# Kernel optimization log

Hardware: AMD Instinct MI355X
Metric: run time of the kernel (lower is better)

## Reference

```python
import jax, jax.numpy as jnp
import numpy as np

B, CIN, CH, COUT = 16, 256, 256, 256
RES = 16
E = 32           # embed_dim
NEMB = 1024      # codebook size
NP = 128         # n_phylo_channels (ch - NP == NP)
L = 4            # n_phylolevels
K = 8            # attribute codes per level per kernel
KN = 32          # nonattribute codes per kernel (levels=1)
CP = L * K * E   # 1024 projected phylo channels
CN = KN * E      # 1024 projected nonattr channels
BETA = 0.25
EPS = 1e-5

def conv1x1(x, w, b):
    # x: [B,C,H,W], w: [O,C], b: [O]
    return jnp.einsum('oc,bchw->bohw', w, x) + b[None, :, None, None]

def layernorm_chw(x, w, b):
    # LayerNorm over (C,H,W) per sample, elementwise affine of shape [C,H,W]
    mu = jnp.mean(x, axis=(1, 2, 3), keepdims=True)
    var = jnp.var(x, axis=(1, 2, 3), keepdims=True)
    return (x - mu) * jax.lax.rsqrt(var + EPS) * w[None] + b[None]

def reshape_in(x, levels):
    # [B, E*levels*K', H, W] -> [B, E, K'*H*W, levels]
    Bb, C, H, W = x.shape
    Kp = C // (E * levels)
    x = x.reshape(Bb, E, levels, Kp, H * W)
    x = x.transpose(0, 1, 3, 4, 2)          # [B,E,K',HW,levels]
    return x.reshape(Bb, E, Kp * H * W, levels)

def reshape_out(x, levels):
    # [B, E, K'*HW, levels] -> [B, E*levels*K', RES, RES]
    Bb, Ee, N, Ll = x.shape
    Kp = N // (RES * RES)
    x = x.reshape(Bb, Ee, Kp, RES * RES, Ll)
    x = x.transpose(0, 1, 4, 2, 3)          # [B,E,levels,K',HW]
    return x.reshape(Bb, Ee * Ll * Kp, RES, RES)

def quantize(z, codebook):
    # z: [B, E, N, levels]; codebook: [NEMB, E]
    zp = z.transpose(0, 2, 3, 1)            # [B,N,levels,E]
    flat = zp.reshape(-1, E)
    d = (jnp.sum(flat * flat, axis=1, keepdims=True)
         - 2.0 * flat @ codebook.T
         + jnp.sum(codebook * codebook, axis=1)[None, :])
    idx = jnp.argmin(d, axis=1)
    zq = codebook[idx].reshape(zp.shape)
    sg = jax.lax.stop_gradient
    loss = jnp.mean((sg(zq) - zp) ** 2) + BETA * jnp.mean((zq - sg(zp)) ** 2)
    zq = zp + sg(zq - zp)                   # straight-through
    return zq.transpose(0, 3, 1, 2), loss

def setup_inputs() -> dict:
    key = jax.random.key(0)
    ks = jax.random.split(key, 20)
    s = 0.02
    inp = {
        'x': jax.random.normal(ks[0], (B, CIN, RES, RES), jnp.float32),
        'conv_in_w': jax.random.normal(ks[1], (CH, CIN), jnp.float32) * s,
        'conv_in_b': jnp.zeros((CH,), jnp.float32),
        'ln_p_w': jnp.ones((NP, RES, RES), jnp.float32),
        'ln_p_b': jnp.zeros((NP, RES, RES), jnp.float32),
        'wp_in': jax.random.normal(ks[2], (CP, NP), jnp.float32) * s,
        'bp_in': jnp.zeros((CP,), jnp.float32),
        'wp_out': jax.random.normal(ks[3], (NP, CP), jnp.float32) * s,
        'bp_out': jnp.zeros((NP,), jnp.float32),
        'ln_n_w': jnp.ones((CH - NP, RES, RES), jnp.float32),
        'ln_n_b': jnp.zeros((CH - NP, RES, RES), jnp.float32),
        'wn_in': jax.random.normal(ks[4], (CN, CH - NP), jnp.float32) * s,
        'bn_in': jnp.zeros((CN,), jnp.float32),
        'wn_out': jax.random.normal(ks[5], (CH - NP, CN), jnp.float32) * s,
        'bn_out': jnp.zeros((CH - NP,), jnp.float32),
        'codebook': jax.random.uniform(ks[6], (NEMB, E), jnp.float32,
                                       -1.0 / NEMB, 1.0 / NEMB),
        'conv_out_w': jax.random.normal(ks[7], (COUT, CH), jnp.float32) * s,
        'conv_out_b': jnp.zeros((COUT,), jnp.float32),
    }
    return inp

def reference(x, conv_in_w, conv_in_b, ln_p_w, ln_p_b, wp_in, bp_in,
              wp_out, bp_out, ln_n_w, ln_n_b, wn_in, bn_in, wn_out, bn_out,
              codebook, conv_out_w, conv_out_b):
    silu = jax.nn.silu
    h = conv1x1(silu(x), conv_in_w, conv_in_b)
    h_p, h_n = h[:, :NP], h[:, NP:]
    # phylo branch
    z_p = silu(conv1x1(layernorm_chw(silu(h_p), ln_p_w, ln_p_b), wp_in, bp_in))
    zq_p, loss_p = quantize(reshape_in(z_p, L), codebook)
    hout_p = silu(conv1x1(reshape_out(zq_p, L), wp_out, bp_out))
    # non-attribute branch (anticlassification path)
    z_n = silu(conv1x1(layernorm_chw(silu(h_n), ln_n_w, ln_n_b), wn_in, bn_in))
    zq_n, loss_n = quantize(reshape_in(z_n, 1), codebook)
    hout_n = silu(conv1x1(reshape_out(zq_n, 1), wn_out, bn_out))
    h_cat = jnp.concatenate([hout_p, hout_n], axis=1)
    out = conv1x1(silu(h_cat), conv_out_w, conv_out_b)
    return out, loss_p + loss_n, zq_p
```

## Files before the change

kernel.cpp:

```cpp
#include <hip/hip_runtime.h>
#include <hip/hip_bf16.h>


__device__ __forceinline__ float silu_rw(float x){ return x / (1.f + expf(-x)); }
__device__ __forceinline__ float b2f_rw(__hip_bfloat16 v){ return __bfloat162float(v); }
__device__ __forceinline__ float ldv_rw(const void* p, int i, int f32m){
  if (f32m) return ((const float*)p)[i];
  return b2f_rw(((const __hip_bfloat16*)p)[i]);
}

#define FLAGS_OFF 0
#define LOSS_OFF  4
#define STATS_OFF 8
#define CB32_OFF  128
#define CBN_OFF   32896
#define IDXP_OFF  33984
#define IDXN_OFF  165056
#define R2_OFF    296192
#define R3_OFF    820480
#define R1_OFF    1344768

__global__ __launch_bounds__(256) void detect_rw(const void* cbv, float* flags, float* lossacc){
  __shared__ int bad;
  if (threadIdx.x == 0) bad = 0;
  __syncthreads();
  const unsigned short* u = (const unsigned short*)cbv;
  int local = 0;
  for (int i = threadIdx.x; i < 32768; i += 256){
    unsigned e = (u[i] >> 7) & 0xFF;
    if (e >= 126) local = 1;
  }
  if (local) bad = 1;
  __syncthreads();
  if (threadIdx.x == 0){
    flags[0] = bad ? 1.f : 0.f;
    lossacc[0] = 0.f; lossacc[1] = 0.f;
  }
}

__global__ __launch_bounds__(256) void cbprep_rw(const void* cbv, const float* flags,
                                                 float* cb32, float* cbn){
  const int f32m = (flags[0] != 0.f);
  int j = blockIdx.x * 256 + threadIdx.x;
  if (j < 1024){
    float s = 0.f;
    for (int e = 0; e < 32; ++e){
      float v = ldv_rw(cbv, j*32 + e, f32m);
      cb32[j*32 + e] = v;
      s += v*v;
    }
    cbn[j] = s;
  }
}

template<int KCH, int INMODE, bool OUTSILU, bool ATOMIC, int LEVELS>
__global__ __launch_bounds__(256) void gemm2_rw(
    const float* __restrict__ inF, const float* __restrict__ inF2,
    const void* __restrict__ inV,
    const void* __restrict__ W, const void* __restrict__ biasO,
    const void* __restrict__ sbA, const void* __restrict__ sbB,
    const int* __restrict__ idxin, const float* __restrict__ cb32,
    float* __restrict__ outF, const float* __restrict__ flags,
    int KDIM, int OUTC, int o_off, int b_base, int ib_sub, int ob_sub)
{
  __shared__ float As[32][32];
  __shared__ float Bs[32][68];
  __shared__ int   IdxS[32][32];

  const int f32m = (flags[0] != 0.f);
  const int t  = threadIdx.x;
  const int q0 = (blockIdx.x << 5) + (b_base << 8);
  const int b  = q0 >> 8;
  const int p0 = q0 & 255;
  const int o0 = blockIdx.y << 6;
  const int k0base = blockIdx.z * KCH;
  const int tx = t & 15, ty = t >> 4;
  float acc[4][2] = {};

  const int sch = t >> 3, spx = (t & 7) << 2;

  if constexpr (INMODE == 3){
    #pragma unroll
    for (int j = 0; j < 4; ++j){
      const int p = p0 + spx + j;
      if constexpr (LEVELS == 4){
        const int l = sch >> 3, kp = sch & 7;
        IdxS[sch][spx + j] = idxin[b*8192 + (((kp << 8) + p) << 2) + l];
      } else {
        IdxS[sch][spx + j] = idxin[b*8192 + (sch << 8) + p];
      }
    }
    __syncthreads();
  }

  for (int kc = 0; kc < KCH; kc += 32){
    const int k0 = k0base + kc;
    if constexpr (INMODE == 0){
      const float4 v = *reinterpret_cast<const float4*>(
          &inF[(((b - ib_sub)*KDIM + k0 + sch) << 8) + p0 + spx]);
      *reinterpret_cast<float4*>(&As[sch][spx]) = v;
    } else if constexpr (INMODE == 2){
      if (f32m){
        const float* xf = (const float*)inV;
        float4 v = *reinterpret_cast<const float4*>(&xf[((b*KDIM + k0 + sch) << 8) + p0 + spx]);
        v.x = silu_rw(v.x); v.y = silu_rw(v.y); v.z = silu_rw(v.z); v.w = silu_rw(v.w);
        *reinterpret_cast<float4*>(&As[sch][spx]) = v;
      } else {
        const __hip_bfloat16* xb = (const __hip_bfloat16*)inV;
        const int off = ((b*KDIM + k0 + sch) << 8) + p0 + spx;
        #pragma unroll
        for (int j = 0; j < 4; ++j) As[sch][spx + j] = silu_rw(b2f_rw(xb[off + j]));
      }
    } else if constexpr (INMODE == 3){
      const int e = k0 >> 5;
      #pragma unroll
      for (int j = 0; j < 4; ++j)
        As[sch][spx + j] = cb32[((IdxS[sch][spx + j] & 1023) << 5) + e];
    } else {
      const float* src = (k0 < 128) ? inF : inF2;
      const void* sb   = (k0 < 128) ? sbA : sbB;
      const int kh = k0 & 127;
      const float bb = ldv_rw(sb, kh + sch, f32m);
      float4 v = *reinterpret_cast<const float4*>(&src[((b*128 + kh + sch) << 8) + p0 + spx]);
      v.x = silu_rw(v.x + bb); v.y = silu_rw(v.y + bb);
      v.z = silu_rw(v.z + bb); v.w = silu_rw(v.w + bb);
      *reinterpret_cast<float4*>(&As[sch][spx]) = v;
    }
    if (f32m){
      const float* Wf = (const float*)W;
      #pragma unroll
      for (int r = 0; r < 8; ++r){
        int ii = t + (r << 8); int oo = ii >> 5, cc = ii & 31;
        Bs[cc][oo] = Wf[(o0 + oo)*KDIM + k0 + cc];
      }
    } else {
      const __hip_bfloat16* Wb = (const __hip_bfloat16*)W;
      #pragma unroll
      for (int r = 0; r < 8; ++r){
        int ii = t + (r << 8); int oo = ii >> 5, cc = ii & 31;
        Bs[cc][oo] = b2f_rw(Wb[(o0 + oo)*KDIM + k0 + cc]);
      }
    }
    __syncthreads();
    #pragma unroll
    for (int kk = 0; kk < 32; ++kk){
      const float2 a = *reinterpret_cast<const float2*>(&As[kk][tx << 1]);
      const float4 w = *reinterpret_cast<const float4*>(&Bs[kk][ty << 2]);
      acc[0][0] += w.x*a.x; acc[0][1] += w.x*a.y;
      acc[1][0] += w.y*a.x; acc[1][1] += w.y*a.y;
      acc[2][0] += w.z*a.x; acc[2][1] += w.z*a.y;
      acc[3][0] += w.w*a.x; acc[3][1] += w.w*a.y;
    }
    __syncthreads();
  }
  #pragma unroll
  for (int i = 0; i < 4; ++i){
    const int o = o0 + (ty << 2) + i;
    const int base = (((b - ob_sub)*OUTC + o_off + o) << 8) + p0 + (tx << 1);
    if constexpr (ATOMIC){
      atomicAdd(&outF[base + 0], acc[i][0]);
      atomicAdd(&outF[base + 1], acc[i][1]);
    } else {
      const float bb = ldv_rw(biasO, o, f32m);
      float v0 = acc[i][0] + bb, v1 = acc[i][1] + bb;
      if constexpr (OUTSILU){ v0 = silu_rw(v0); v1 = silu_rw(v1); }
      *reinterpret_cast<float2*>(&outF[base]) = make_float2(v0, v1);
    }
  }
}

__global__ __launch_bounds__(256) void stats_rw(const float* __restrict__ h, float* __restrict__ stats){
  const int b = blockIdx.x >> 1, half = blockIdx.x & 1;
  const float* base = h + ((b*256 + half*128) << 8);
  float s = 0.f, s2 = 0.f;
  for (int i = threadIdx.x; i < 32768; i += 256){
    float a = silu_rw(base[i]);
    s += a; s2 += a*a;
  }
  __shared__ float sh[2][256];
  sh[0][threadIdx.x] = s; sh[1][threadIdx.x] = s2;
  __syncthreads();
  for (int st = 128; st > 0; st >>= 1){
    if (threadIdx.x < st){
      sh[0][threadIdx.x] += sh[0][threadIdx.x + st];
      sh[1][threadIdx.x] += sh[1][threadIdx.x + st];
    }
    __syncthreads();
  }
  if (threadIdx.x == 0){
    float mu  = sh[0][0] * (1.f/32768.f);
    float var = sh[1][0] * (1.f/32768.f) - mu*mu;
    stats[half*32 + b]      = mu;
    stats[half*32 + 16 + b] = 1.f / sqrtf(var + 1e-5f);
  }
}

__global__ __launch_bounds__(256) void ln_rw(const float* __restrict__ h,
    const void* lwp, const void* lbp, const void* lwn, const void* lbn,
    const float* __restrict__ stats, const float* __restrict__ flags,
    float* __restrict__ lnp, float* __restrict__ lnn){
  const int f32m = (flags[0] != 0.f);
  int i = blockIdx.x * 256 + threadIdx.x;
  int b = i >> 16, c = (i >> 8) & 255, p = i & 255;
  float a = silu_rw(h[i]);
  if (c < 128){
    float v = (a - stats[b]) * stats[16 + b] * ldv_rw(lwp, (c << 8) + p, f32m) + ldv_rw(lbp, (c << 8) + p, f32m);
    lnp[((b*128 + c) << 8) + p] = v;
  } else {
    int cc = c - 128;
    float v = (a - stats[32 + b]) * stats[48 + b] * ldv_rw(lwn, (cc << 8) + p, f32m) + ldv_rw(lbn, (cc << 8) + p, f32m);
    lnn[((b*128 + cc) << 8) + p] = v;
  }
}

template<int LEVELS>
__global__ __launch_bounds__(256) void quant_rw(const float* __restrict__ z,
    const float* __restrict__ cb32, const float* __restrict__ cbn,
    int* __restrict__ idxout, float* __restrict__ lossacc, int b_base, int CS){
  __shared__ float4 cbT[2056];
  __shared__ float  cbnS[1056];
  __shared__ float  red[256];

  const int tid = threadIdx.x;
  const int gid = blockIdx.x * 256 + tid;
  const int pt = gid & 7;
  const int vbase = gid >> 3;
  const int halfstride = CS << 12;
  const int vid0 = vbase, vid1 = vbase + halfstride;

  const int bl0 = vid0 >> 13, bl1 = vid1 >> 13;
  const int w = vid0 & 8191;
  int p, cbase;
  if (LEVELS == 4){
    int l = w & 3, n = w >> 2;
    p = n & 255; cbase = (l << 3) + (n >> 8);
  } else {
    p = w & 255; cbase = w >> 8;
  }

  #pragma unroll
  for (int q = 0; q < 4; ++q){
    const int i = tid + (q << 8);
    cbnS[i + (i >> 5)] = cbn[i];
  }

  float4 za[8], zb[8];
  float zn0 = 0.f, zn1 = 0.f;
  const int zoff = ((bl0 << 10) + cbase) << 8;
  const int zoff1 = ((bl1 << 10) + cbase) << 8;
  #pragma unroll
  for (int e4 = 0; e4 < 8; ++e4){
    float4 a, b;
    a.x = z[zoff  + (((e4<<2)+0) << 13) + p];
    a.y = z[zoff  + (((e4<<2)+1) << 13) + p];
    a.z = z[zoff  + (((e4<<2)+2) << 13) + p];
    a.w = z[zoff  + (((e4<<2)+3) << 13) + p];
    b.x = z[zoff1 + (((e4<<2)+0) << 13) + p];
    b.y = z[zoff1 + (((e4<<2)+1) << 13) + p];
    b.z = z[zoff1 + (((e4<<2)+2) << 13) + p];
    b.w = z[zoff1 + (((e4<<2)+3) << 13) + p];
    za[e4] = a; zb[e4] = b;
    zn0 += a.x*a.x; zn0 += a.y*a.y; zn0 += a.z*a.z; zn0 += a.w*a.w;
    zn1 += b.x*b.x; zn1 += b.y*b.y; zn1 += b.z*b.z; zn1 += b.w*b.w;
  }

  float best0 = __builtin_inff(), best1 = __builtin_inff();
  int bi0 = 0, bi1 = 0;

  const int jl0 = pt << 5;
  for (int t = 0; t < 4; ++t){
    __syncthreads();
    const float4* g4 = reinterpret_cast<const float4*>(cb32) + (t << 11);
    #pragma unroll
    for (int r = 0; r < 8; ++r){
      const int idx = tid + (r << 8);
      cbT[idx + (idx >> 8)] = g4[idx];
    }
    __syncthreads();

    #pragma unroll 4
    for (int i = 0; i < 32; ++i){
      const int jl = jl0 + i;
      const int j  = (t << 8) + jl;
      const float4* c = &cbT[(jl << 3) + (jl >> 5)];
      float dot0 = 0.f, dot1 = 0.f;
      #pragma unroll
      for (int e4 = 0; e4 < 8; ++e4){
        const float4 cc = c[e4];
        dot0 = fmaf(za[e4].x, cc.x, dot0); dot1 = fmaf(zb[e4].x, cc.x, dot1);
        dot0 = fmaf(za[e4].y, cc.y, dot0); dot1 = fmaf(zb[e4].y, cc.y, dot1);
        dot0 = fmaf(za[e4].z, cc.z, dot0); dot1 = fmaf(zb[e4].z, cc.z, dot1);
        dot0 = fmaf(za[e4].w, cc.w, dot0); dot1 = fmaf(zb[e4].w, cc.w, dot1);
      }
      const float cn = cbnS[j + (j >> 5)];
      const float d0 = (zn0 - 2.f*dot0) + cn;
      const float d1 = (zn1 - 2.f*dot1) + cn;
      if (d0 < best0){ best0 = d0; bi0 = j; }
      if (d1 < best1){ best1 = d1; bi1 = j; }
    }
  }

  #pragma unroll
  for (int k = 4; k > 0; k >>= 1){
    float od0 = __shfl_down(best0, k); int oj0 = __shfl_down(bi0, k);
    float od1 = __shfl_down(best1, k); int oj1 = __shfl_down(bi1, k);
    if (od0 < best0 || (od0 == best0 && oj0 < bi0)){ best0 = od0; bi0 = oj0; }
    if (od1 < best1 || (od1 == best1 && oj1 < bi1)){ best1 = od1; bi1 = oj1; }
  }
  if (pt == 0){
    idxout[(b_base + bl0)*8192 + w] = bi0;
    idxout[(b_base + bl1)*8192 + w] = bi1;
  }
  red[tid] = (pt == 0) ? (best0 + best1) : 0.f;
  __syncthreads();
  for (int st = 128; st > 0; st >>= 1){
    if (tid < st) red[tid] += red[tid + st];
    __syncthreads();
  }
  if (tid == 0) atomicAdd(lossacc, red[0]);
}

__global__ __launch_bounds__(256) void zqout_rw(const int* __restrict__ idxp,
    const float* __restrict__ cb32, float* __restrict__ out){
  int t = blockIdx.x * 256 + threadIdx.x;
  int l = t & 3, n = (t >> 2) & 2047, e = (t >> 13) & 31, b = t >> 18;
  int id = idxp[b*8192 + (n << 2) + l];
  out[t] = cb32[((id & 1023) << 5) + e];
}

__global__ __launch_bounds__(256) void zero_rw(float* __restrict__ p){
  p[blockIdx.x * 256 + threadIdx.x] = 0.f;
}

__global__ void loss_rw(const float* __restrict__ lossacc, float* __restrict__ out){
  if (threadIdx.x == 0 && blockIdx.x == 0)
    out[0] = 1.25f * (lossacc[0] + lossacc[1]) * (1.f/4194304.f);
}

extern "C" void kernel_launch(void* const* d_in, const int* in_sizes, int n_in,
                              void* d_out, int out_size, void* d_ws, size_t ws_size,
                              hipStream_t stream){
  (void)in_sizes; (void)n_in; (void)out_size;
  const void* x   = d_in[0];
  const void* ciw = d_in[1];
  const void* cib = d_in[2];
  const void* lwp = d_in[3];
  const void* lbp = d_in[4];
  const void* wpi = d_in[5];
  const void* bpi = d_in[6];
  const void* wpo = d_in[7];
  const void* bpo = d_in[8];
  const void* lwn = d_in[9];
  const void* lbn = d_in[10];
  const void* wni = d_in[11];
  const void* bni = d_in[12];
  const void* wno = d_in[13];
  const void* bno = d_in[14];
  const void* cbk = d_in[15];
  const void* cow = d_in[16];
  const void* cob = d_in[17];

  float* ws    = (float*)d_ws;
  float* flags = ws + FLAGS_OFF;
  float* loss  = ws + LOSS_OFF;
  float* stats = ws + STATS_OFF;
  float* cb32  = ws + CB32_OFF;
  float* cbn   = ws + CBN_OFF;
  int*   idxp  = (int*)(ws + IDXP_OFF);
  int*   idxn  = (int*)(ws + IDXN_OFF);
  float* R2    = ws + R2_OFF;
  float* R3    = ws + R3_OFF;
  float* R1    = ws + R1_OFF;

  float* outO = (float*)d_out;
  float* outL = outO + 1048576;
  float* outZ = outO + 1048577;

  const size_t wsf = ws_size / 4;
  int CS = 4;
  if      (wsf >= (size_t)R1_OFF + 16u*262144u) CS = 16;
  else if (wsf >= (size_t)R1_OFF +  8u*262144u) CS = 8;

  detect_rw<<<1, 256, 0, stream>>>(cbk, flags, loss);
  cbprep_rw<<<4, 256, 0, stream>>>(cbk, flags, cb32, cbn);
  gemm2_rw<256,2,false,false,0><<<dim3(128,4), 256, 0, stream>>>(
      nullptr, nullptr, x, ciw, cib, nullptr, nullptr, nullptr, nullptr,
      R1, flags, 256, 256, 0, 0, 0, 0);
  stats_rw<<<32, 256, 0, stream>>>(R1, stats);
  ln_rw<<<4096, 256, 0, stream>>>(R1, lwp, lbp, lwn, lbn, stats, flags, R2, R3);
  for (int c = 0; c < 16; c += CS){
    gemm2_rw<128,0,true,false,0><<<dim3(CS*8,16), 256, 0, stream>>>(
        R2, nullptr, nullptr, wpi, bpi, nullptr, nullptr, nullptr, nullptr,
        R1, flags, 128, 1024, 0, c, 0, c);
    quant_rw<4><<<CS*128, 256, 0, stream>>>(R1, cb32, cbn, idxp, loss + 0, c, CS);
  }
  for (int c = 0; c < 16; c += CS){
    gemm2_rw<128,0,true,false,0><<<dim3(CS*8,16), 256, 0, stream>>>(
        R3, nullptr, nullptr, wni, bni, nullptr, nullptr, nullptr, nullptr,
        R1, flags, 128, 1024, 0, c, 0, c);
    quant_rw<1><<<CS*128, 256, 0, stream>>>(R1, cb32, cbn, idxn, loss + 1, c, CS);
  }
  zqout_rw<<<16384, 256, 0, stream>>>(idxp, cb32, outZ);
  zero_rw<<<4096, 256, 0, stream>>>(R2);
  gemm2_rw<256,3,false,true,4><<<dim3(128,2,4), 256, 0, stream>>>(
      nullptr, nullptr, nullptr, wpo, nullptr, nullptr, nullptr, idxp, cb32,
      R2, flags, 1024, 128, 0, 0, 0, 0);
  gemm2_rw<256,3,false,true,1><<<dim3(128,2,4), 256, 0, stream>>>(
      nullptr, nullptr, nullptr, wno, nullptr, nullptr, nullptr, idxn, cb32,
      R3, flags, 1024, 128, 0, 0, 0, 0);
  gemm2_rw<256,5,false,false,0><<<dim3(128,4), 256, 0, stream>>>(
      R2, R3, nullptr, cow, cob, bpo, bno, nullptr, nullptr,
      outO, flags, 256, 256, 0, 0, 0, 0);
  loss_rw<<<1, 64, 0, stream>>>(loss, outL);
}
```

Before: 636.7 us.

## Compute VQ distances with split-bf16 MFMA and exact fp32 fallback for ties

Replaces the scalar fp32 codebook distance search with MFMA 16x16x32 bf16 matrix ops, using a hi/lo bf16 split (three products) to approximate fp32 dot products. It tracks the best and second-best distance per vector. Vectors whose margin falls below an error bound are pushed to a list and recomputed exactly in fp32 by a fallback kernel. This targets the dominant ALU cost of the quantizer, at the price of extra launches, atomics and a correctness dependence on the error bound.

```diff
diff --git a/kernel.cpp b/kernel.cpp
--- a/kernel.cpp
+++ b/kernel.cpp
@@ -1,6 +1,9 @@
 #include <hip/hip_runtime.h>
 #include <hip/hip_bf16.h>
 
+
+typedef float f32x4  __attribute__((ext_vector_type(4)));
+typedef short bf16x8 __attribute__((ext_vector_type(8)));
 
 __device__ __forceinline__ float silu_rw(float x){ return x / (1.f + expf(-x)); }
 __device__ __forceinline__ float b2f_rw(__hip_bfloat16 v){ return __bfloat162float(v); }
@@ -8,19 +11,32 @@
   if (f32m) return ((const float*)p)[i];
   return b2f_rw(((const __hip_bfloat16*)p)[i]);
 }
+__device__ __forceinline__ unsigned short f2bf_rw(float x){
+  unsigned u = __float_as_uint(x);
+  unsigned r = ((u >> 16) & 1u) + 0x7FFFu;
+  return (unsigned short)((u + r) >> 16);
+}
+__device__ __forceinline__ float bf2f_rw(unsigned short h){
+  return __uint_as_float(((unsigned)h) << 16);
+}
 
 #define FLAGS_OFF 0
 #define LOSS_OFF  4
 #define STATS_OFF 8
+#define CNT_OFF   72
+#define CMAX_OFF  80
 #define CB32_OFF  128
 #define CBN_OFF   32896
 #define IDXP_OFF  33984
 #define IDXN_OFF  165056
-#define R2_OFF    296192
-#define R3_OFF    820480
-#define R1_OFF    1344768
-
-__global__ __launch_bounds__(256) void detect_rw(const void* cbv, float* flags, float* lossacc){
+#define CBH_OFF   296192
+#define CBL_OFF   312576
+#define LIST_OFF  328960
+#define R2_OFF    460032
+#define R3_OFF    984320
+#define R1_OFF    1508608
+
+__global__ __launch_bounds__(256) void detect_rw(const void* cbv, float* wsb){
   __shared__ int bad;
   if (threadIdx.x == 0) bad = 0;
   __syncthreads();
@@ -33,13 +49,18 @@
   if (local) bad = 1;
   __syncthreads();
   if (threadIdx.x == 0){
-    flags[0] = bad ? 1.f : 0.f;
-    lossacc[0] = 0.f; lossacc[1] = 0.f;
+    wsb[FLAGS_OFF] = bad ? 1.f : 0.f;
+    wsb[LOSS_OFF] = 0.f; wsb[LOSS_OFF + 1] = 0.f;
+    int* c = (int*)(wsb + CNT_OFF);
+    #pragma unroll
+    for (int k = 0; k < 8; ++k) c[k] = 0;
+    wsb[CMAX_OFF] = 0.f;
   }
 }
 
 __global__ __launch_bounds__(256) void cbprep_rw(const void* cbv, const float* flags,
-                                                 float* cb32, float* cbn){
+                                                 float* cb32, float* cbn,
+                                                 short* cbh, short* cbl, float* cmaxp){
   const int f32m = (flags[0] != 0.f);
   int j = blockIdx.x * 256 + threadIdx.x;
   if (j < 1024){
@@ -47,9 +68,13 @@
     for (int e = 0; e < 32; ++e){
       float v = ldv_rw(cbv, j*32 + e, f32m);
       cb32[j*32 + e] = v;
+      unsigned short h = f2bf_rw(v);
+      cbh[j*32 + e] = (short)h;
+      cbl[j*32 + e] = (short)f2bf_rw(v - bf2f_rw(h));
       s += v*v;
     }
     cbn[j] = s;
+    atomicMax((int*)cmaxp, __float_as_int(sqrtf(s)));
   }
 }
 
@@ -214,110 +239,167 @@
 }
 
 template<int LEVELS>
-__global__ __launch_bounds__(256) void quant_rw(const float* __restrict__ z,
-    const float* __restrict__ cb32, const float* __restrict__ cbn,
-    int* __restrict__ idxout, float* __restrict__ lossacc, int b_base, int CS){
-  __shared__ float4 cbT[2056];
-  __shared__ float  cbnS[1056];
-  __shared__ float  red[256];
-
-  const int tid = threadIdx.x;
-  const int gid = blockIdx.x * 256 + tid;
-  const int pt = gid & 7;
-  const int vbase = gid >> 3;
-  const int halfstride = CS << 12;
-  const int vid0 = vbase, vid1 = vbase + halfstride;
-
-  const int bl0 = vid0 >> 13, bl1 = vid1 >> 13;
-  const int w = vid0 & 8191;
-  int p, cbase;
-  if (LEVELS == 4){
-    int l = w & 3, n = w >> 2;
-    p = n & 255; cbase = (l << 3) + (n >> 8);
-  } else {
-    p = w & 255; cbase = w >> 8;
-  }
-
+__global__ __launch_bounds__(256) void quantm_rw(
+    const float* __restrict__ z, const short* __restrict__ cbh,
+    const short* __restrict__ cbl, const float* __restrict__ cbn,
+    const float* __restrict__ cmaxp, int* __restrict__ idxout,
+    float* __restrict__ lossacc, int* __restrict__ cnt,
+    int* __restrict__ list, int b_base)
+{
+  const int tid  = threadIdx.x;
+  const int lane = tid & 63, wid = tid >> 6;
+  const int lc = lane & 15, gq = lane >> 4;
+  const int bid  = blockIdx.x;
+  const int bl   = bid >> 6;
+  const int rest = bid & 63;
+  const int g = rest >> 1, half = rest & 1;
+  int cb, wbase, wstep;
+  if (LEVELS == 4){ cb = (g & 3)*8 + (g >> 2); wbase = (g >> 2)*1024 + (g & 3); wstep = 4; }
+  else            { cb = g;                    wbase = g << 8;                  wstep = 1; }
+  const int pb = half*128 + wid*32;
+
+  bf16x8 ah0, al0, ah1, al1;
+  float zn0 = 0.f, zn1 = 0.f;
+  const int zoff = (((bl << 10) + cb) << 8) + pb + lc;
+  const int e0 = gq << 3;
   #pragma unroll
-  for (int q = 0; q < 4; ++q){
-    const int i = tid + (q << 8);
-    cbnS[i + (i >> 5)] = cbn[i];
-  }
-
-  float4 za[8], zb[8];
-  float zn0 = 0.f, zn1 = 0.f;
-  const int zoff = ((bl0 << 10) + cbase) << 8;
-  const int zoff1 = ((bl1 << 10) + cbase) << 8;
+  for (int i = 0; i < 8; ++i){
+    const int zo = zoff + ((e0 + i) << 13);
+    const float z0 = z[zo];
+    const float z1 = z[zo + 16];
+    zn0 += z0*z0; zn1 += z1*z1;
+    const float s0 = -2.f*z0, s1 = -2.f*z1;
+    const unsigned short h0 = f2bf_rw(s0);
+    const unsigned short h1 = f2bf_rw(s1);
+    ah0[i] = (short)h0; al0[i] = (short)f2bf_rw(s0 - bf2f_rw(h0));
+    ah1[i] = (short)h1; al1[i] = (short)f2bf_rw(s1 - bf2f_rw(h1));
+  }
+  zn0 += __shfl_xor(zn0, 16); zn0 += __shfl_xor(zn0, 32);
+  zn1 += __shfl_xor(zn1, 16); zn1 += __shfl_xor(zn1, 32);
+
+  float m1[8], m2[8]; int j1[8];
   #pragma unroll
-  for (int e4 = 0; e4 < 8; ++e4){
-    float4 a, b;
-    a.x = z[zoff  + (((e4<<2)+0) << 13) + p];
-    a.y = z[zoff  + (((e4<<2)+1) << 13) + p];
-    a.z = z[zoff  + (((e4<<2)+2) << 13) + p];
-    a.w = z[zoff  + (((e4<<2)+3) << 13) + p];
-    b.x = z[zoff1 + (((e4<<2)+0) << 13) + p];
-    b.y = z[zoff1 + (((e4<<2)+1) << 13) + p];
-    b.z = z[zoff1 + (((e4<<2)+2) << 13) + p];
-    b.w = z[zoff1 + (((e4<<2)+3) << 13) + p];
-    za[e4] = a; zb[e4] = b;
-    zn0 += a.x*a.x; zn0 += a.y*a.y; zn0 += a.z*a.z; zn0 += a.w*a.w;
-    zn1 += b.x*b.x; zn1 += b.y*b.y; zn1 += b.z*b.z; zn1 += b.w*b.w;
-  }
-
-  float best0 = __builtin_inff(), best1 = __builtin_inff();
-  int bi0 = 0, bi1 = 0;
-
-  const int jl0 = pt << 5;
-  for (int t = 0; t < 4; ++t){
-    __syncthreads();
-    const float4* g4 = reinterpret_cast<const float4*>(cb32) + (t << 11);
-    #pragma unroll
-    for (int r = 0; r < 8; ++r){
-      const int idx = tid + (r << 8);
-      cbT[idx + (idx >> 8)] = g4[idx];
-    }
-    __syncthreads();
-
-    #pragma unroll 4
-    for (int i = 0; i < 32; ++i){
-      const int jl = jl0 + i;
-      const int j  = (t << 8) + jl;
-      const float4* c = &cbT[(jl << 3) + (jl >> 5)];
-      float dot0 = 0.f, dot1 = 0.f;
+  for (int s = 0; s < 8; ++s){ m1[s] = __builtin_inff(); m2[s] = __builtin_inff(); j1[s] = 0; }
+
+  const short* bhp = cbh + (lc << 5) + e0;
+  const short* blp = cbl + (lc << 5) + e0;
+  const float* cnp = cbn + lc;
+
+  #pragma unroll 2
+  for (int t = 0; t < 64; ++t){
+    const int j0 = t << 4;
+    const bf16x8 bh  = *reinterpret_cast<const bf16x8*>(bhp + (j0 << 5));
+    const bf16x8 blo = *reinterpret_cast<const bf16x8*>(blp + (j0 << 5));
+    const float cnv = cnp[j0];
+    f32x4 a0 = {cnv, cnv, cnv, cnv};
+    f32x4 a1 = {cnv, cnv, cnv, cnv};
+    a0 = __builtin_amdgcn_mfma_f32_16x16x32_bf16(ah0, bh,  a0, 0, 0, 0);
+    a0 = __builtin_amdgcn_mfma_f32_16x16x32_bf16(ah0, blo, a0, 0, 0, 0);
+    a0 = __builtin_amdgcn_mfma_f32_16x16x32_bf16(al0, bh,  a0, 0, 0, 0);
+    a1 = __builtin_amdgcn_mfma_f32_16x16x32_bf16(ah1, bh,  a1, 0, 0, 0);
+    a1 = __builtin_amdgcn_mfma_f32_16x16x32_bf16(ah1, blo, a1, 0, 0, 0);
+    a1 = __builtin_amdgcn_mfma_f32_16x16x32_bf16(al1, bh,  a1, 0, 0, 0);
+    const int jc = j0 + lc;
+    #pragma unroll
+    for (int r = 0; r < 4; ++r){
+      const float d0 = a0[r];
+      m2[r] = fminf(m2[r], fmaxf(m1[r], d0));
+      const bool t0 = d0 < m1[r];
+      j1[r] = t0 ? jc : j1[r]; m1[r] = t0 ? d0 : m1[r];
+      const float d1 = a1[r];
+      m2[4+r] = fminf(m2[4+r], fmaxf(m1[4+r], d1));
+      const bool t1 = d1 < m1[4+r];
+      j1[4+r] = t1 ? jc : j1[4+r]; m1[4+r] = t1 ? d1 : m1[4+r];
+    }
+  }
+
+  #pragma unroll
+  for (int k = 1; k < 16; k <<= 1){
+    #pragma unroll
+    for (int s = 0; s < 8; ++s){
+      const float om1 = __shfl_xor(m1[s], k);
+      const float om2 = __shfl_xor(m2[s], k);
+      const int   oj  = __shfl_xor(j1[s], k);
+      m2[s] = fminf(fminf(m2[s], om2), fmaxf(m1[s], om1));
+      const bool tk = (om1 < m1[s]) || (om1 == m1[s] && oj < j1[s]);
+      m1[s] = tk ? om1 : m1[s];
+      j1[s] = tk ? oj  : j1[s];
+    }
+  }
+
+  const float cmax = cmaxp[0];
+  float lossw = 0.f;
+  #pragma unroll
+  for (int f = 0; f < 2; ++f){
+    #pragma unroll
+    for (int r = 0; r < 4; ++r){
+      const int s = f*4 + r;
+      const int vrow = (gq << 2) + r;
+      const float znv = __shfl(f == 0 ? zn0 : zn1, vrow);
+      if (lc == 0){
+        const int p  = pb + f*16 + vrow;
+        const int gi = (b_base + bl)*8192 + wbase + p*wstep;
+        idxout[gi] = j1[s];
+        const float eb = fmaf(2.0e-6f, znv, 3.0e-4f * sqrtf(znv) * cmax);
+        if (m2[s] - m1[s] > eb){
+          lossw += znv + m1[s];
+        } else {
+          const int pos = atomicAdd(cnt, 1);
+          list[pos] = (((bl << 5) | g) << 8) | p;
+        }
+      }
+    }
+  }
+  lossw += __shfl_xor(lossw, 16);
+  lossw += __shfl_xor(lossw, 32);
+  if (lane == 0) atomicAdd(lossacc, lossw);
+}
+
+template<int LEVELS>
+__global__ __launch_bounds__(256) void fb_rw(
+    const float* __restrict__ z, const float* __restrict__ cb32,
+    const float* __restrict__ cbn, const int* __restrict__ cnt,
+    const int* __restrict__ list, int* __restrict__ idxout,
+    float* __restrict__ lossacc, int b_base)
+{
+  const int lane = threadIdx.x & 63;
+  const int wv = (blockIdx.x << 2) | (threadIdx.x >> 6);
+  const int n = cnt[0];
+  for (int it = wv; it < n; it += 256){
+    const int id = list[it];
+    const int p = id & 255, g = (id >> 8) & 31, bl = id >> 13;
+    int cb, w;
+    if (LEVELS == 4){ cb = (g & 3)*8 + (g >> 2); w = (g >> 2)*1024 + (p << 2) + (g & 3); }
+    else            { cb = g;                    w = (g << 8) + p; }
+    const int zoff = (((bl << 10) + cb) << 8) + p;
+    float myz = 0.f;
+    if (lane < 32) myz = z[zoff + (lane << 13)];
+    float zn = 0.f;
+    #pragma unroll
+    for (int e = 0; e < 32; ++e){
+      const float v = __shfl(myz, e);
+      zn = fmaf(v, v, zn);
+    }
+    float bd = __builtin_inff(); int bj = 0;
+    for (int j = lane; j < 1024; j += 64){
+      const float* c = cb32 + (j << 5);
+      float dot = 0.f;
       #pragma unroll
-      for (int e4 = 0; e4 < 8; ++e4){
-        const float4 cc = c[e4];
-        dot0 = fmaf(za[e4].x, cc.x, dot0); dot1 = fmaf(zb[e4].x, cc.x, dot1);
-        dot0 = fmaf(za[e4].y, cc.y, dot0); dot1 = fmaf(zb[e4].y, cc.y, dot1);
-        dot0 = fmaf(za[e4].z, cc.z, dot0); dot1 = fmaf(zb[e4].z, cc.z, dot1);
-        dot0 = fmaf(za[e4].w, cc.w, dot0); dot1 = fmaf(zb[e4].w, cc.w, dot1);
-      }
-      const float cn = cbnS[j + (j >> 5)];
-      const float d0 = (zn0 - 2.f*dot0) + cn;
-      const float d1 = (zn1 - 2.f*dot1) + cn;
-      if (d0 < best0){ best0 = d0; bi0 = j; }
-      if (d1 < best1){ best1 = d1; bi1 = j; }
-    }
-  }
-
-  #pragma unroll
-  for (int k = 4; k > 0; k >>= 1){
-    float od0 = __shfl_down(best0, k); int oj0 = __shfl_down(bi0, k);
-    float od1 = __shfl_down(best1, k); int oj1 = __shfl_down(bi1, k);
-    if (od0 < best0 || (od0 == best0 && oj0 < bi0)){ best0 = od0; bi0 = oj0; }
-    if (od1 < best1 || (od1 == best1 && oj1 < bi1)){ best1 = od1; bi1 = oj1; }
-  }
-  if (pt == 0){
-    idxout[(b_base + bl0)*8192 + w] = bi0;
-    idxout[(b_base + bl1)*8192 + w] = bi1;
-  }
-  red[tid] = (pt == 0) ? (best0 + best1) : 0.f;
-  __syncthreads();
-  for (int st = 128; st > 0; st >>= 1){
-    if (tid < st) red[tid] += red[tid + st];
-    __syncthreads();
-  }
-  if (tid == 0) atomicAdd(lossacc, red[0]);
+      for (int e = 0; e < 32; ++e) dot = fmaf(__shfl(myz, e), c[e], dot);
+      const float d = (zn - 2.f*dot) + cbn[j];
+      if (d < bd){ bd = d; bj = j; }
+    }
+    #pragma unroll
+    for (int k = 1; k < 64; k <<= 1){
+      const float od = __shfl_xor(bd, k);
+      const int   oj = __shfl_xor(bj, k);
+      if (od < bd || (od == bd && oj < bj)){ bd = od; bj = oj; }
+    }
+    if (lane == 0){
+      idxout[(b_base + bl)*8192 + w] = bj;
+      atomicAdd(lossacc, bd);
+    }
+  }
 }
 
 __global__ __launch_bounds__(256) void zqout_rw(const int* __restrict__ idxp,
@@ -364,10 +446,15 @@
   float* flags = ws + FLAGS_OFF;
   float* loss  = ws + LOSS_OFF;
   float* stats = ws + STATS_OFF;
+  float* cmaxp = ws + CMAX_OFF;
   float* cb32  = ws + CB32_OFF;
   float* cbn   = ws + CBN_OFF;
+  int*   cnts  = (int*)(ws + CNT_OFF);
   int*   idxp  = (int*)(ws + IDXP_OFF);
   int*   idxn  = (int*)(ws + IDXN_OFF);
+  short* cbh   = (short*)(ws + CBH_OFF);
+  short* cbl   = (short*)(ws + CBL_OFF);
+  int*   list  = (int*)(ws + LIST_OFF);
   float* R2    = ws + R2_OFF;
   float* R3    = ws + R3_OFF;
   float* R1    = ws + R1_OFF;
@@ -381,24 +468,36 @@
   if      (wsf >= (size_t)R1_OFF + 16u*262144u) CS = 16;
   else if (wsf >= (size_t)R1_OFF +  8u*262144u) CS = 8;
 
-  detect_rw<<<1, 256, 0, stream>>>(cbk, flags, loss);
-  cbprep_rw<<<4, 256, 0, stream>>>(cbk, flags, cb32, cbn);
+  detect_rw<<<1, 256, 0, stream>>>(cbk, ws);
+  cbprep_rw<<<4, 256, 0, stream>>>(cbk, flags, cb32, cbn, cbh, cbl, cmaxp);
   gemm2_rw<256,2,false,false,0><<<dim3(128,4), 256, 0, stream>>>(
       nullptr, nullptr, x, ciw, cib, nullptr, nullptr, nullptr, nullptr,
       R1, flags, 256, 256, 0, 0, 0, 0);
   stats_rw<<<32, 256, 0, stream>>>(R1, stats);
   ln_rw<<<4096, 256, 0, stream>>>(R1, lwp, lbp, lwn, lbn, stats, flags, R2, R3);
-  for (int c = 0; c < 16; c += CS){
-    gemm2_rw<128,0,true,false,0><<<dim3(CS*8,16), 256, 0, stream>>>(
-        R2, nullptr, nullptr, wpi, bpi, nullptr, nullptr, nullptr, nullptr,
-        R1, flags, 128, 1024, 0, c, 0, c);
-    quant_rw<4><<<CS*128, 256, 0, stream>>>(R1, cb32, cbn, idxp, loss + 0, c, CS);
-  }
-  for (int c = 0; c < 16; c += CS){
-    gemm2_rw<128,0,true,false,0><<<dim3(CS*8,16), 256, 0, stream>>>(
-        R3, nullptr, nullptr, wni, bni, nullptr, nullptr, nullptr, nullptr,
-        R1, flags, 128, 1024, 0, c, 0, c);
-    quant_rw<1><<<CS*128, 256, 0, stream>>>(R1, cb32, cbn, idxn, loss + 1, c, CS);
+  {
+    int ci = 0;
+    for (int c = 0; c < 16; c += CS, ++ci){
+      gemm2_rw<128,0,true,false,0><<<dim3(CS*8,16), 256, 0, stream>>>(
+          R2, nullptr, nullptr, wpi, bpi, nullptr, nullptr, nullptr, nullptr,
+          R1, flags, 128, 1024, 0, c, 0, c);
+      quantm_rw<4><<<CS*64, 256, 0, stream>>>(R1, cbh, cbl, cbn, cmaxp,
+                                              idxp, loss + 0, cnts + ci, list, c);
+      fb_rw<4><<<64, 256, 0, stream>>>(R1, cb32, cbn, cnts + ci, list,
+                                       idxp, loss + 0, c);
+    }
+  }
+  {
+    int ci = 4;
+    for (int c = 0; c < 16; c += CS, ++ci){
+      gemm2_rw<128,0,true,false,0><<<dim3(CS*8,16), 256, 0, stream>>>(
+          R3, nullptr, nullptr, wni, bni, nullptr, nullptr, nullptr, nullptr,
+          R1, flags, 128, 1024, 0, c, 0, c);
+      quantm_rw<1><<<CS*64, 256, 0, stream>>>(R1, cbh, cbl, cbn, cmaxp,
+                                              idxn, loss + 1, cnts + ci, list, c);
+      fb_rw<1><<<64, 256, 0, stream>>>(R1, cb32, cbn, cnts + ci, list,
+                                       idxn, loss + 1, c);
+    }
   }
   zqout_rw<<<16384, 256, 0, stream>>>(idxp, cb32, outZ);
   zero_rw<<<4096, 256, 0, stream>>>(R2);
```

Result: slower. 683.4 us (+7.3%).
